# Performance work log

Hardware: AMD Instinct MI355X
Metric: run time of the kernel (lower is better)

The kernel has to match this reference:

```python
import jax, jax.numpy as jnp
import numpy as np

N_EXPERTS = 8
Z_DIM = 128
HID = 1024
OUT = 3072  # e.g. 3x32x32 flattened generator output
BATCH = 2048


def hash_vectors(z, n):
    """Deterministic per-sample hash -> expert index in [0, n).

    Proxy for the repo's hash_vectors (which hashes the latent vector):
    quantize |z|, sum over feature dim, mod n. Non-differentiable by design.
    """
    return jnp.mod(jnp.floor(jnp.abs(z) * 1000.0).sum(axis=1).astype(jnp.int32), n)


def setup_inputs() -> dict:
    key = jax.random.key(0)
    kz, k1, kb1, k2, kb2 = jax.random.split(key, 5)
    z = jax.random.normal(kz, (BATCH, Z_DIM), dtype=jnp.float32)
    s1 = 1.0 / np.sqrt(Z_DIM)
    s2 = 1.0 / np.sqrt(HID)
    # Stacked per-expert MLP params (each expert independently initialized,
    # mirroring reset_parameters on each deepcopy).
    W1 = jax.random.uniform(k1, (N_EXPERTS, Z_DIM, HID), jnp.float32, -s1, s1)
    b1 = jax.random.uniform(kb1, (N_EXPERTS, HID), jnp.float32, -s1, s1)
    W2 = jax.random.uniform(k2, (N_EXPERTS, HID, OUT), jnp.float32, -s2, s2)
    b2 = jax.random.uniform(kb2, (N_EXPERTS, OUT), jnp.float32, -s2, s2)
    return {"z": z, "W1": W1, "b1": b1, "W2": W2, "b2": b2}


def reference(z, W1, b1, W2, b2):
    # Hard routing: each sample i goes to expert idx[i].
    idx = hash_vectors(z, N_EXPERTS)  # [B]
    # Dense compute-all-experts then select (vectorized replacement for the
    # per-sample Python loop in the original forward).
    h = jax.nn.relu(jnp.einsum('bi,eih->beh', z, W1) + b1[None, :, :])  # [B,E,H]
    y = jnp.einsum('beh,eho->beo', h, W2) + b2[None, :, :]              # [B,E,O]
    out = jnp.take_along_axis(y, idx[:, None, None], axis=1)[:, 0, :]   # [B,O]
    return out
```

## Files before the change

kernel.cpp:

```cpp
#include <hip/hip_runtime.h>
#include <hip/hip_bf16.h>


#define BATCH 2048
#define ZD 128
#define HID 1024
#define OUTD 3072
#define NEXP 8

#define TMG 128
#define TNG 128
#define BKG 64
#define MAXTF 24

typedef short bf16x8 __attribute__((ext_vector_type(8)));
typedef float f32x4 __attribute__((ext_vector_type(4)));


__global__ __launch_bounds__(256) void route_kernel(const float* __restrict__ z,
                                                    __hip_bfloat16* __restrict__ zb,
                                                    int* counts, int* bucket) {
    __shared__ int lcnt[NEXP];
    __shared__ int gbase[NEXP];
    int t = threadIdx.x;
    if (t < NEXP) lcnt[t] = 0;
    __syncthreads();

    int s = blockIdx.x * 32 + (t >> 3);
    int li = t & 7;
    const float* zp = z + (size_t)s * ZD + li * 16;
    float sum = 0.f;
    union { bf16x8 v8; __hip_bfloat16 h[8]; } u0, u1;
#pragma unroll
    for (int i = 0; i < 4; i++) {
        float4 v = ((const float4*)zp)[i];
        sum += floorf(fabsf(v.x) * 1000.0f) + floorf(fabsf(v.y) * 1000.0f) +
               floorf(fabsf(v.z) * 1000.0f) + floorf(fabsf(v.w) * 1000.0f);
        __hip_bfloat16* dst = (i < 2) ? &u0.h[i * 4] : &u1.h[(i - 2) * 4];
        dst[0] = __float2bfloat16(v.x);
        dst[1] = __float2bfloat16(v.y);
        dst[2] = __float2bfloat16(v.z);
        dst[3] = __float2bfloat16(v.w);
    }
    bf16x8* zo = (bf16x8*)(zb + (size_t)s * ZD + li * 16);
    zo[0] = u0.v8;
    zo[1] = u1.v8;

    sum += __shfl_down(sum, 4);
    sum += __shfl_down(sum, 2);
    sum += __shfl_down(sum, 1);
    int e = 0, lpos = 0;
    if (li == 0) {
        e = ((int)sum) & 7;
        lpos = atomicAdd(&lcnt[e], 1);
    }
    __syncthreads();
    if (t < NEXP) gbase[t] = atomicAdd(&counts[t], lcnt[t]);
    __syncthreads();
    if (li == 0) bucket[e * BATCH + gbase[e] + lpos] = s;
}

__global__ void scan_kernel(const int* __restrict__ counts, int* ntl,
                            int* texp, int* perm, const int* __restrict__ bucket) {
    __shared__ int soff[NEXP + 1];
    __shared__ int scnt[NEXP];
    if (threadIdx.x == 0) {
        int o = 0;
        for (int e = 0; e < NEXP; e++) {
            scnt[e] = counts[e];
            soff[e] = o;
            o += (scnt[e] + TMG - 1) & ~(TMG - 1);
        }
        soff[NEXP] = o;
        *ntl = o / TMG;
    }
    __syncthreads();
    int total = soff[NEXP];
    for (int r = threadIdx.x; r < total; r += blockDim.x) {
        int e = 0;
        while (r >= soff[e + 1]) e++;
        int i = r - soff[e];
        perm[r] = (i < scnt[e]) ? bucket[e * BATCH + i] : -1;
        if ((r & (TMG - 1)) == 0) texp[r / TMG] = e;
    }
}

__global__ __launch_bounds__(256, 3) void gemm1_fast(
    const __hip_bfloat16* __restrict__ zb, const float* __restrict__ W1,
    const float* __restrict__ b1, const int* __restrict__ ntl,
    const int* __restrict__ texp, const int* __restrict__ perm,
    __hip_bfloat16* __restrict__ H) {
    int mt = blockIdx.y;
    if (mt >= *ntl) return;
    int e = texp[mt];
    int n0 = blockIdx.x * TNG;

    __shared__ __align__(16) __hip_bfloat16 As[TMG * BKG];
    __shared__ __align__(16) __hip_bfloat16 Bs[TNG * BKG];
    __shared__ int rows_s[TMG];

    int tid = threadIdx.x;
    if (tid < TMG) rows_s[tid] = perm[mt * TMG + tid];
    __syncthreads();

    int lane = tid & 63, wave = tid >> 6;
    int cc = lane & 15, q = lane >> 4;
    int mw = (wave >> 1) * 64, nw = (wave & 1) * 64;

    int sr = tid >> 3, sc = tid & 7;
    int awbase = sr * 64 + (sc ^ (sr & 7)) * 8;
    const __hip_bfloat16* Arp[4];
#pragma unroll
    for (int p = 0; p < 4; p++) {
        int r = rows_s[p * 32 + sr];
        if (r < 0) r = 0;
        Arp[p] = zb + (size_t)r * ZD + sc * 8;
    }
    int bkc = tid & 7, bn = (tid >> 3) * 4;
    const float* Bgf = W1 + (size_t)e * ZD * HID + (size_t)(bkc * 8) * HID + n0 + bn;
    int bwb[4];
#pragma unroll
    for (int j = 0; j < 4; j++)
        bwb[j] = (bn + j) * 64 + ((bkc ^ ((bn + j) & 7))) * 8;

    int A0 = (mw + cc) * 64, B0 = (nw + cc) * 64;
    int X0 = (q ^ (cc & 7)) * 8, X1 = ((4 + q) ^ (cc & 7)) * 8;

    float bias[4];
#pragma unroll
    for (int j = 0; j < 4; j++) bias[j] = b1[(size_t)e * HID + n0 + nw + j * 16 + cc];

    f32x4 zero4 = {0.f, 0.f, 0.f, 0.f};
    f32x4 acc[4][4];
#pragma unroll
    for (int i = 0; i < 4; i++)
#pragma unroll
        for (int j = 0; j < 4; j++) acc[i][j] = zero4;

    bf16x8 ga[4];
    union { bf16x8 v8; __hip_bfloat16 h[8]; } gb[4];
#pragma unroll
    for (int p = 0; p < 4; p++) ga[p] = *(const bf16x8*)(Arp[p]);
#pragma unroll
    for (int i = 0; i < 8; i++) {
        float4 v = *(const float4*)(Bgf + (size_t)i * HID);
        gb[0].h[i] = __float2bfloat16(v.x);
        gb[1].h[i] = __float2bfloat16(v.y);
        gb[2].h[i] = __float2bfloat16(v.z);
        gb[3].h[i] = __float2bfloat16(v.w);
    }
#pragma unroll
    for (int it = 0; it < ZD / BKG; ++it) {
        __syncthreads();
#pragma unroll
        for (int p = 0; p < 4; p++) *(bf16x8*)(As + awbase + p * 2048) = ga[p];
#pragma unroll
        for (int j = 0; j < 4; j++) *(bf16x8*)(Bs + bwb[j]) = gb[j].v8;
        __syncthreads();
        if (it + 1 < ZD / BKG) {
#pragma unroll
            for (int p = 0; p < 4; p++)
                ga[p] = *(const bf16x8*)(Arp[p] + (it + 1) * BKG);
#pragma unroll
            for (int i = 0; i < 8; i++) {
                float4 v = *(const float4*)(Bgf + (size_t)((it + 1) * BKG + i) * HID);
                gb[0].h[i] = __float2bfloat16(v.x);
                gb[1].h[i] = __float2bfloat16(v.y);
                gb[2].h[i] = __float2bfloat16(v.z);
                gb[3].h[i] = __float2bfloat16(v.w);
            }
        }
#pragma unroll
        for (int kh = 0; kh < 2; ++kh) {
            int X = kh ? X1 : X0;
            bf16x8 af[4], bfr[4];
#pragma unroll
            for (int i = 0; i < 4; i++) af[i] = *(const bf16x8*)(As + A0 + i * 1024 + X);
#pragma unroll
            for (int j = 0; j < 4; j++) bfr[j] = *(const bf16x8*)(Bs + B0 + j * 1024 + X);
#pragma unroll
            for (int i = 0; i < 4; i++)
#pragma unroll
                for (int j = 0; j < 4; j++)
                    acc[i][j] = __builtin_amdgcn_mfma_f32_16x16x32_bf16(af[i], bfr[j],
                                                                        acc[i][j], 0, 0, 0);
        }
    }
#pragma unroll
    for (int i = 0; i < 4; i++)
#pragma unroll
        for (int r = 0; r < 4; r++) {
            int m = mw + i * 16 + q * 4 + r;
            __hip_bfloat16* hp = H + (size_t)(mt * TMG + m) * HID + n0 + nw + cc;
#pragma unroll
            for (int j = 0; j < 4; j++)
                hp[j * 16] = __float2bfloat16(fmaxf(acc[i][j][r] + bias[j], 0.f));
        }
}

__global__ __launch_bounds__(256, 2) void gemm2_fast(
    const __hip_bfloat16* __restrict__ H, const float* __restrict__ W2,
    const float* __restrict__ b2, const int* __restrict__ ntl,
    const int* __restrict__ texp, const int* __restrict__ perm,
    float* __restrict__ out) {
    int mt = blockIdx.y;
    if (mt >= *ntl) return;
    int e = texp[mt];
    int n0 = blockIdx.x * TNG;

    __shared__ __align__(16) __hip_bfloat16 As[2][TMG * BKG];
    __shared__ __align__(16) __hip_bfloat16 Bs[2][TNG * BKG];
    __shared__ int rows_s[TMG];

    int tid = threadIdx.x;
    if (tid < TMG) rows_s[tid] = perm[mt * TMG + tid];

    int lane = tid & 63, wave = tid >> 6;
    int cc = lane & 15, q = lane >> 4;
    int mw = (wave >> 1) * 64, nw = (wave & 1) * 64;

    int sr = tid >> 3, sc = tid & 7;
    int awbase = sr * 64 + (sc ^ (sr & 7)) * 8;
    const __hip_bfloat16* Ag = H + ((size_t)mt * TMG + sr) * HID + sc * 8;
    int bkc = tid & 7, bn = (tid >> 3) * 4;
    const float* Bgf = W2 + (size_t)e * HID * OUTD + (size_t)(bkc * 8) * OUTD + n0 + bn;
    int bwb[4];
#pragma unroll
    for (int j = 0; j < 4; j++)
        bwb[j] = (bn + j) * 64 + ((bkc ^ ((bn + j) & 7))) * 8;

    int A0 = (mw + cc) * 64, B0 = (nw + cc) * 64;
    int X0 = (q ^ (cc & 7)) * 8, X1 = ((4 + q) ^ (cc & 7)) * 8;

    float bias[4];
#pragma unroll
    for (int j = 0; j < 4; j++) bias[j] = b2[(size_t)e * OUTD + n0 + nw + j * 16 + cc];

    f32x4 zero4 = {0.f, 0.f, 0.f, 0.f};
    f32x4 acc[4][4];
#pragma unroll
    for (int i = 0; i < 4; i++)
#pragma unroll
        for (int j = 0; j < 4; j++) acc[i][j] = zero4;

    bf16x8 ga[4];
    float4 braw[8];
#pragma unroll
    for (int p = 0; p < 4; p++) ga[p] = *(const bf16x8*)(Ag + (size_t)p * 32 * HID);
#pragma unroll
    for (int i = 0; i < 8; i++) braw[i] = *(const float4*)(Bgf + (size_t)i * OUTD);

    const int NIT = HID / BKG;
    for (int it = 0; it < NIT; ++it) {
        __hip_bfloat16* Ac = As[it & 1];
        __hip_bfloat16* Bc = Bs[it & 1];
        union { bf16x8 v8; __hip_bfloat16 h[8]; } gb[4];
#pragma unroll
        for (int i = 0; i < 8; i++) {
            gb[0].h[i] = __float2bfloat16(braw[i].x);
            gb[1].h[i] = __float2bfloat16(braw[i].y);
            gb[2].h[i] = __float2bfloat16(braw[i].z);
            gb[3].h[i] = __float2bfloat16(braw[i].w);
        }
#pragma unroll
        for (int p = 0; p < 4; p++) *(bf16x8*)(Ac + awbase + p * 2048) = ga[p];
#pragma unroll
        for (int j = 0; j < 4; j++) *(bf16x8*)(Bc + bwb[j]) = gb[j].v8;
        if (it + 1 < NIT) {
            int k1 = (it + 1) * BKG;
#pragma unroll
            for (int p = 0; p < 4; p++)
                ga[p] = *(const bf16x8*)(Ag + (size_t)p * 32 * HID + k1);
#pragma unroll
            for (int i = 0; i < 8; i++)
                braw[i] = *(const float4*)(Bgf + (size_t)(k1 + i) * OUTD);
        }
        __syncthreads();
#pragma unroll
        for (int kh = 0; kh < 2; ++kh) {
            int X = kh ? X1 : X0;
            bf16x8 af[4], bfr[4];
#pragma unroll
            for (int i = 0; i < 4; i++) af[i] = *(const bf16x8*)(Ac + A0 + i * 1024 + X);
#pragma unroll
            for (int j = 0; j < 4; j++) bfr[j] = *(const bf16x8*)(Bc + B0 + j * 1024 + X);
#pragma unroll
            for (int i = 0; i < 4; i++)
#pragma unroll
                for (int j = 0; j < 4; j++)
                    acc[i][j] = __builtin_amdgcn_mfma_f32_16x16x32_bf16(af[i], bfr[j],
                                                                        acc[i][j], 0, 0, 0);
        }
    }
#pragma unroll
    for (int i = 0; i < 4; i++)
#pragma unroll
        for (int r = 0; r < 4; r++) {
            int m = mw + i * 16 + q * 4 + r;
            int orow = rows_s[m];
            if (orow >= 0) {
                float* op = out + (size_t)orow * OUTD + n0 + nw + cc;
#pragma unroll
                for (int j = 0; j < 4; j++) op[j * 16] = acc[i][j][r] + bias[j];
            }
        }
}

extern "C" void kernel_launch(void* const* d_in, const int* in_sizes, int n_in,
                              void* d_out, int out_size, void* d_ws, size_t ws_size,
                              hipStream_t stream) {
    const float* z  = (const float*)d_in[0];
    const float* W1 = (const float*)d_in[1];
    const float* b1 = (const float*)d_in[2];
    const float* W2 = (const float*)d_in[3];
    const float* b2 = (const float*)d_in[4];
    float* out = (float*)d_out;

    char* ws = (char*)d_ws;
    int* counts = (int*)ws;
    int* ntl    = (int*)(ws + 64);
    int* texp   = (int*)(ws + 128);
    int* perm   = (int*)(ws + 256);
    int* bucket = (int*)(ws + 12544);
    __hip_bfloat16* zb  = (__hip_bfloat16*)(ws + 78080);
    __hip_bfloat16* Hb  = (__hip_bfloat16*)(ws + 602368);

    hipMemsetAsync(counts, 0, 64, stream);
    hipLaunchKernelGGL(route_kernel, dim3(BATCH / 32), dim3(256), 0, stream,
                       z, zb, counts, bucket);
    hipLaunchKernelGGL(scan_kernel, dim3(1), dim3(256), 0, stream,
                       counts, ntl, texp, perm, bucket);
    hipLaunchKernelGGL(gemm1_fast, dim3(HID / TNG, MAXTF), dim3(256), 0, stream,
                       zb, W1, b1, ntl, texp, perm, Hb);
    hipLaunchKernelGGL(gemm2_fast, dim3(OUTD / TNG, MAXTF), dim3(256), 0, stream,
                       Hb, W2, b2, ntl, texp, perm, out);
}
```

Before: 202.4 us.

## Deepen gemm2 global-load prefetch to two stages of register buffers

Restructures the gemm2 main loop to hold two sets of register prefetch buffers and issue global loads two K-iterations ahead, unrolling the loop by two via a macro. The aim is to hide more global memory latency behind MFMA work. It roughly doubles the registers used for prefetch (ga and braw), which under launch_bounds(256,2) may cause spills or lower occupancy.

```diff
diff --git a/kernel.cpp b/kernel.cpp
--- a/kernel.cpp
+++ b/kernel.cpp
@@ -198,6 +198,49 @@
         }
 }
 
+#define PIPE(S, IT)                                                            \
+    {                                                                          \
+        __hip_bfloat16* Ac = As[S];                                           \
+        __hip_bfloat16* Bc = Bs[S];                                           \
+        union { bf16x8 v8; __hip_bfloat16 h[8]; } gbv[4];                     \
+        _Pragma("unroll")                                                      \
+        for (int i = 0; i < 8; i++) {                                          \
+            gbv[0].h[i] = __float2bfloat16(braw[S][i].x);                      \
+            gbv[1].h[i] = __float2bfloat16(braw[S][i].y);                      \
+            gbv[2].h[i] = __float2bfloat16(braw[S][i].z);                      \
+            gbv[3].h[i] = __float2bfloat16(braw[S][i].w);                      \
+        }                                                                      \
+        _Pragma("unroll")                                                      \
+        for (int p = 0; p < 4; p++) *(bf16x8*)(Ac + awbase + p * 2048) = ga[S][p]; \
+        _Pragma("unroll")                                                      \
+        for (int j = 0; j < 4; j++) *(bf16x8*)(Bc + bwb[j]) = gbv[j].v8;       \
+        if ((IT) + 2 < NIT) {                                                  \
+            int k2 = ((IT) + 2) * BKG;                                         \
+            _Pragma("unroll")                                                  \
+            for (int p = 0; p < 4; p++)                                        \
+                ga[S][p] = *(const bf16x8*)(Ag + (size_t)p * 32 * HID + k2);   \
+            _Pragma("unroll")                                                  \
+            for (int i = 0; i < 8; i++)                                        \
+                braw[S][i] = *(const float4*)(Bgf + (size_t)(k2 + i) * OUTD);  \
+        }                                                                      \
+        __syncthreads();                                                       \
+        _Pragma("unroll")                                                      \
+        for (int kh = 0; kh < 2; ++kh) {                                       \
+            int X = kh ? X1 : X0;                                              \
+            bf16x8 af[4], bfr[4];                                              \
+            _Pragma("unroll")                                                  \
+            for (int i = 0; i < 4; i++) af[i] = *(const bf16x8*)(Ac + A0 + i * 1024 + X); \
+            _Pragma("unroll")                                                  \
+            for (int j = 0; j < 4; j++) bfr[j] = *(const bf16x8*)(Bc + B0 + j * 1024 + X); \
+            _Pragma("unroll")                                                  \
+            for (int i = 0; i < 4; i++)                                        \
+                _Pragma("unroll")                                              \
+                for (int j = 0; j < 4; j++)                                    \
+                    acc[i][j] = __builtin_amdgcn_mfma_f32_16x16x32_bf16(       \
+                        af[i], bfr[j], acc[i][j], 0, 0, 0);                    \
+        }                                                                      \
+    }
+
 __global__ __launch_bounds__(256, 2) void gemm2_fast(
     const __hip_bfloat16* __restrict__ H, const float* __restrict__ W2,
     const float* __restrict__ b2, const int* __restrict__ ntl,
@@ -243,55 +286,25 @@
 #pragma unroll
         for (int j = 0; j < 4; j++) acc[i][j] = zero4;
 
-    bf16x8 ga[4];
-    float4 braw[8];
-#pragma unroll
-    for (int p = 0; p < 4; p++) ga[p] = *(const bf16x8*)(Ag + (size_t)p * 32 * HID);
-#pragma unroll
-    for (int i = 0; i < 8; i++) braw[i] = *(const float4*)(Bgf + (size_t)i * OUTD);
-
     const int NIT = HID / BKG;
-    for (int it = 0; it < NIT; ++it) {
-        __hip_bfloat16* Ac = As[it & 1];
-        __hip_bfloat16* Bc = Bs[it & 1];
-        union { bf16x8 v8; __hip_bfloat16 h[8]; } gb[4];
-#pragma unroll
-        for (int i = 0; i < 8; i++) {
-            gb[0].h[i] = __float2bfloat16(braw[i].x);
-            gb[1].h[i] = __float2bfloat16(braw[i].y);
-            gb[2].h[i] = __float2bfloat16(braw[i].z);
-            gb[3].h[i] = __float2bfloat16(braw[i].w);
-        }
-#pragma unroll
-        for (int p = 0; p < 4; p++) *(bf16x8*)(Ac + awbase + p * 2048) = ga[p];
-#pragma unroll
-        for (int j = 0; j < 4; j++) *(bf16x8*)(Bc + bwb[j]) = gb[j].v8;
-        if (it + 1 < NIT) {
-            int k1 = (it + 1) * BKG;
-#pragma unroll
-            for (int p = 0; p < 4; p++)
-                ga[p] = *(const bf16x8*)(Ag + (size_t)p * 32 * HID + k1);
-#pragma unroll
-            for (int i = 0; i < 8; i++)
-                braw[i] = *(const float4*)(Bgf + (size_t)(k1 + i) * OUTD);
-        }
-        __syncthreads();
-#pragma unroll
-        for (int kh = 0; kh < 2; ++kh) {
-            int X = kh ? X1 : X0;
-            bf16x8 af[4], bfr[4];
-#pragma unroll
-            for (int i = 0; i < 4; i++) af[i] = *(const bf16x8*)(Ac + A0 + i * 1024 + X);
-#pragma unroll
-            for (int j = 0; j < 4; j++) bfr[j] = *(const bf16x8*)(Bc + B0 + j * 1024 + X);
-#pragma unroll
-            for (int i = 0; i < 4; i++)
-#pragma unroll
-                for (int j = 0; j < 4; j++)
-                    acc[i][j] = __builtin_amdgcn_mfma_f32_16x16x32_bf16(af[i], bfr[j],
-                                                                        acc[i][j], 0, 0, 0);
-        }
-    }
+
+    bf16x8 ga[2][4];
+    float4 braw[2][8];
+#pragma unroll
+    for (int s = 0; s < 2; s++) {
+#pragma unroll
+        for (int p = 0; p < 4; p++)
+            ga[s][p] = *(const bf16x8*)(Ag + (size_t)p * 32 * HID + s * BKG);
+#pragma unroll
+        for (int i = 0; i < 8; i++)
+            braw[s][i] = *(const float4*)(Bgf + (size_t)(s * BKG + i) * OUTD);
+    }
+
+    for (int it = 0; it < NIT; it += 2) {
+        PIPE(0, it);
+        PIPE(1, it + 1);
+    }
+
 #pragma unroll
     for (int i = 0; i < 4; i++)
 #pragma unroll
```

New measurement: 203.9 us. About the same (+0.7%).

## Shrink GEMM N tiles, warp-specialize loaders, double-buffer gemm1 shared memory

Applied to the files above, without the earlier changes.

Both grouped GEMMs use narrower N tiles: 32 columns for gemm1 and 64 for gemm2. This launches more blocks so more of the GPU is busy given the small routed M. Loading is split by wave: some waves fetch and convert W to bf16 while others fetch the gathered activations. gemm1 also gets double-buffered shared memory, and the occupancy hints are raised. The cost is more redundant A reloads, since each A tile is now fetched by more blocks, plus lower MFMA reuse per block and idle waves during loads.

```diff
diff --git a/kernel.cpp b/kernel.cpp
--- a/kernel.cpp
+++ b/kernel.cpp
@@ -7,10 +7,6 @@
 #define HID 1024
 #define OUTD 3072
 #define NEXP 8
-
-#define TMG 128
-#define TNG 128
-#define BKG 64
 #define MAXTF 24
 
 typedef short bf16x8 __attribute__((ext_vector_type(8)));
@@ -69,10 +65,10 @@
         for (int e = 0; e < NEXP; e++) {
             scnt[e] = counts[e];
             soff[e] = o;
-            o += (scnt[e] + TMG - 1) & ~(TMG - 1);
+            o += (scnt[e] + 127) & ~127;
         }
         soff[NEXP] = o;
-        *ntl = o / TMG;
+        *ntl = o / 128;
     }
     __syncthreads();
     int total = soff[NEXP];
@@ -81,11 +77,11 @@
         while (r >= soff[e + 1]) e++;
         int i = r - soff[e];
         perm[r] = (i < scnt[e]) ? bucket[e * BATCH + i] : -1;
-        if ((r & (TMG - 1)) == 0) texp[r / TMG] = e;
-    }
-}
-
-__global__ __launch_bounds__(256, 3) void gemm1_fast(
+        if ((r & 127) == 0) texp[r / 128] = e;
+    }
+}
+
+__global__ __launch_bounds__(256, 4) void gemm1_fast(
     const __hip_bfloat16* __restrict__ zb, const float* __restrict__ W1,
     const float* __restrict__ b1, const int* __restrict__ ntl,
     const int* __restrict__ texp, const int* __restrict__ perm,
@@ -93,97 +89,102 @@
     int mt = blockIdx.y;
     if (mt >= *ntl) return;
     int e = texp[mt];
-    int n0 = blockIdx.x * TNG;
-
-    __shared__ __align__(16) __hip_bfloat16 As[TMG * BKG];
-    __shared__ __align__(16) __hip_bfloat16 Bs[TNG * BKG];
-    __shared__ int rows_s[TMG];
+    int n0 = blockIdx.x * 32;
+
+    __shared__ __align__(16) __hip_bfloat16 As[2][128 * 64];
+    __shared__ __align__(16) __hip_bfloat16 Bs[2][32 * 64];
+    __shared__ int rows_s[128];
 
     int tid = threadIdx.x;
-    if (tid < TMG) rows_s[tid] = perm[mt * TMG + tid];
+    if (tid < 128) rows_s[tid] = perm[mt * 128 + tid];
     __syncthreads();
 
     int lane = tid & 63, wave = tid >> 6;
     int cc = lane & 15, q = lane >> 4;
-    int mw = (wave >> 1) * 64, nw = (wave & 1) * 64;
-
-    int sr = tid >> 3, sc = tid & 7;
-    int awbase = sr * 64 + (sc ^ (sr & 7)) * 8;
-    const __hip_bfloat16* Arp[4];
-#pragma unroll
-    for (int p = 0; p < 4; p++) {
-        int r = rows_s[p * 32 + sr];
+    int mw = (wave >> 1) * 64, nw = (wave & 1) * 16;
+
+    bool isB = (wave == 0);
+    bool isA = (wave >= 2);
+    int bkc = tid & 7, bn = ((tid >> 3) & 7) * 4;
+    const float* Bgf = W1 + (size_t)e * ZD * HID + (size_t)(bkc * 8) * HID + n0 + bn;
+    int bwb[4];
+#pragma unroll
+    for (int j = 0; j < 4; j++)
+        bwb[j] = ((bn + j) * 8 + (bkc ^ ((bn + j) & 7))) * 8;
+    int t2 = tid & 127;
+    int sc = t2 & 7, rg = t2 >> 3;
+    const __hip_bfloat16* Arp[8];
+#pragma unroll
+    for (int p = 0; p < 8; p++) {
+        int r = rows_s[rg + 16 * p];
         if (r < 0) r = 0;
         Arp[p] = zb + (size_t)r * ZD + sc * 8;
     }
-    int bkc = tid & 7, bn = (tid >> 3) * 4;
-    const float* Bgf = W1 + (size_t)e * ZD * HID + (size_t)(bkc * 8) * HID + n0 + bn;
-    int bwb[4];
-#pragma unroll
-    for (int j = 0; j < 4; j++)
-        bwb[j] = (bn + j) * 64 + ((bkc ^ ((bn + j) & 7))) * 8;
+    int awb = rg * 64 + (sc ^ (rg & 7)) * 8;
 
     int A0 = (mw + cc) * 64, B0 = (nw + cc) * 64;
     int X0 = (q ^ (cc & 7)) * 8, X1 = ((4 + q) ^ (cc & 7)) * 8;
 
-    float bias[4];
-#pragma unroll
-    for (int j = 0; j < 4; j++) bias[j] = b1[(size_t)e * HID + n0 + nw + j * 16 + cc];
+    float bias = b1[(size_t)e * HID + n0 + nw + cc];
 
     f32x4 zero4 = {0.f, 0.f, 0.f, 0.f};
-    f32x4 acc[4][4];
-#pragma unroll
-    for (int i = 0; i < 4; i++)
-#pragma unroll
-        for (int j = 0; j < 4; j++) acc[i][j] = zero4;
-
-    bf16x8 ga[4];
-    union { bf16x8 v8; __hip_bfloat16 h[8]; } gb[4];
-#pragma unroll
-    for (int p = 0; p < 4; p++) ga[p] = *(const bf16x8*)(Arp[p]);
-#pragma unroll
-    for (int i = 0; i < 8; i++) {
-        float4 v = *(const float4*)(Bgf + (size_t)i * HID);
-        gb[0].h[i] = __float2bfloat16(v.x);
-        gb[1].h[i] = __float2bfloat16(v.y);
-        gb[2].h[i] = __float2bfloat16(v.z);
-        gb[3].h[i] = __float2bfloat16(v.w);
-    }
-#pragma unroll
-    for (int it = 0; it < ZD / BKG; ++it) {
+    f32x4 acc[4];
+#pragma unroll
+    for (int i = 0; i < 4; i++) acc[i] = zero4;
+
+    float4 braw[8];
+    bf16x8 ga[8];
+    if (isB) {
+#pragma unroll
+        for (int i = 0; i < 8; i++) braw[i] = *(const float4*)(Bgf + (size_t)i * HID);
+    } else if (isA) {
+#pragma unroll
+        for (int p = 0; p < 8; p++) ga[p] = *(const bf16x8*)(Arp[p]);
+    }
+
+    const int NIT = ZD / 64;
+#pragma unroll
+    for (int it = 0; it < NIT; ++it) {
+        __hip_bfloat16* Ac = As[it & 1];
+        __hip_bfloat16* Bc = Bs[it & 1];
+        if (isB) {
+            union { bf16x8 v8; __hip_bfloat16 h[8]; } gbv[4];
+#pragma unroll
+            for (int i = 0; i < 8; i++) {
+                gbv[0].h[i] = __float2bfloat16(braw[i].x);
+                gbv[1].h[i] = __float2bfloat16(braw[i].y);
+                gbv[2].h[i] = __float2bfloat16(braw[i].z);
+                gbv[3].h[i] = __float2bfloat16(braw[i].w);
+            }
+#pragma unroll
+            for (int j = 0; j < 4; j++) *(bf16x8*)(Bc + bwb[j]) = gbv[j].v8;
+        } else if (isA) {
+#pragma unroll
+            for (int p = 0; p < 8; p++) *(bf16x8*)(Ac + awb + p * 1024) = ga[p];
+        }
+        if (it + 1 < NIT) {
+            int k1 = (it + 1) * 64;
+            if (isB) {
+#pragma unroll
+                for (int i = 0; i < 8; i++)
+                    braw[i] = *(const float4*)(Bgf + (size_t)(k1 + i) * HID);
+            } else if (isA) {
+#pragma unroll
+                for (int p = 0; p < 8; p++) ga[p] = *(const bf16x8*)(Arp[p] + k1);
+            }
+        }
         __syncthreads();
-#pragma unroll
-        for (int p = 0; p < 4; p++) *(bf16x8*)(As + awbase + p * 2048) = ga[p];
-#pragma unroll
-        for (int j = 0; j < 4; j++) *(bf16x8*)(Bs + bwb[j]) = gb[j].v8;
-        __syncthreads();
-        if (it + 1 < ZD / BKG) {
-#pragma unroll
-            for (int p = 0; p < 4; p++)
-                ga[p] = *(const bf16x8*)(Arp[p] + (it + 1) * BKG);
-#pragma unroll
-            for (int i = 0; i < 8; i++) {
-                float4 v = *(const float4*)(Bgf + (size_t)((it + 1) * BKG + i) * HID);
-                gb[0].h[i] = __float2bfloat16(v.x);
-                gb[1].h[i] = __float2bfloat16(v.y);
-                gb[2].h[i] = __float2bfloat16(v.z);
-                gb[3].h[i] = __float2bfloat16(v.w);
-            }
-        }
 #pragma unroll
         for (int kh = 0; kh < 2; ++kh) {
             int X = kh ? X1 : X0;
-            bf16x8 af[4], bfr[4];
-#pragma unroll
-            for (int i = 0; i < 4; i++) af[i] = *(const bf16x8*)(As + A0 + i * 1024 + X);
-#pragma unroll
-            for (int j = 0; j < 4; j++) bfr[j] = *(const bf16x8*)(Bs + B0 + j * 1024 + X);
+            bf16x8 af[4], bfr;
+#pragma unroll
+            for (int i = 0; i < 4; i++) af[i] = *(const bf16x8*)(Ac + A0 + i * 1024 + X);
+            bfr = *(const bf16x8*)(Bc + B0 + X);
 #pragma unroll
             for (int i = 0; i < 4; i++)
-#pragma unroll
-                for (int j = 0; j < 4; j++)
-                    acc[i][j] = __builtin_amdgcn_mfma_f32_16x16x32_bf16(af[i], bfr[j],
-                                                                        acc[i][j], 0, 0, 0);
+                acc[i] = __builtin_amdgcn_mfma_f32_16x16x32_bf16(af[i], bfr,
+                                                                 acc[i], 0, 0, 0);
         }
     }
 #pragma unroll
@@ -191,14 +192,12 @@
 #pragma unroll
         for (int r = 0; r < 4; r++) {
             int m = mw + i * 16 + q * 4 + r;
-            __hip_bfloat16* hp = H + (size_t)(mt * TMG + m) * HID + n0 + nw + cc;
-#pragma unroll
-            for (int j = 0; j < 4; j++)
-                hp[j * 16] = __float2bfloat16(fmaxf(acc[i][j][r] + bias[j], 0.f));
-        }
-}
-
-__global__ __launch_bounds__(256, 2) void gemm2_fast(
+            H[(size_t)(mt * 128 + m) * HID + n0 + nw + cc] =
+                __float2bfloat16(fmaxf(acc[i][r] + bias, 0.f));
+        }
+}
+
+__global__ __launch_bounds__(256, 3) void gemm2_fast(
     const __hip_bfloat16* __restrict__ H, const float* __restrict__ W2,
     const float* __restrict__ b2, const int* __restrict__ ntl,
     const int* __restrict__ texp, const int* __restrict__ perm,
@@ -206,88 +205,98 @@
     int mt = blockIdx.y;
     if (mt >= *ntl) return;
     int e = texp[mt];
-    int n0 = blockIdx.x * TNG;
-
-    __shared__ __align__(16) __hip_bfloat16 As[2][TMG * BKG];
-    __shared__ __align__(16) __hip_bfloat16 Bs[2][TNG * BKG];
-    __shared__ int rows_s[TMG];
+    int n0 = blockIdx.x * 64;
+
+    __shared__ __align__(16) __hip_bfloat16 As[2][128 * 64];
+    __shared__ __align__(16) __hip_bfloat16 Bs[2][64 * 64];
+    __shared__ int rows_s[128];
 
     int tid = threadIdx.x;
-    if (tid < TMG) rows_s[tid] = perm[mt * TMG + tid];
-
+    if (tid < 128) rows_s[tid] = perm[mt * 128 + tid];
     int lane = tid & 63, wave = tid >> 6;
     int cc = lane & 15, q = lane >> 4;
-    int mw = (wave >> 1) * 64, nw = (wave & 1) * 64;
-
-    int sr = tid >> 3, sc = tid & 7;
-    int awbase = sr * 64 + (sc ^ (sr & 7)) * 8;
-    const __hip_bfloat16* Ag = H + ((size_t)mt * TMG + sr) * HID + sc * 8;
-    int bkc = tid & 7, bn = (tid >> 3) * 4;
+    int mw = (wave >> 1) * 64, nw = (wave & 1) * 32;
+
+    bool isB = (wave < 2);
+    int bkc = tid & 7, bn = ((tid >> 3) & 15) * 4;
     const float* Bgf = W2 + (size_t)e * HID * OUTD + (size_t)(bkc * 8) * OUTD + n0 + bn;
     int bwb[4];
 #pragma unroll
     for (int j = 0; j < 4; j++)
-        bwb[j] = (bn + j) * 64 + ((bkc ^ ((bn + j) & 7))) * 8;
+        bwb[j] = ((bn + j) * 8 + (bkc ^ ((bn + j) & 7))) * 8;
+    int t2 = tid & 127;
+    int sc = t2 & 7, rg = t2 >> 3;
+    const __hip_bfloat16* Ag = H + ((size_t)mt * 128 + rg) * HID + sc * 8;
+    int awb = rg * 64 + (sc ^ (rg & 7)) * 8;
 
     int A0 = (mw + cc) * 64, B0 = (nw + cc) * 64;
     int X0 = (q ^ (cc & 7)) * 8, X1 = ((4 + q) ^ (cc & 7)) * 8;
 
-    float bias[4];
-#pragma unroll
-    for (int j = 0; j < 4; j++) bias[j] = b2[(size_t)e * OUTD + n0 + nw + j * 16 + cc];
+    float bias[2];
+#pragma unroll
+    for (int j = 0; j < 2; j++) bias[j] = b2[(size_t)e * OUTD + n0 + nw + j * 16 + cc];
 
     f32x4 zero4 = {0.f, 0.f, 0.f, 0.f};
-    f32x4 acc[4][4];
+    f32x4 acc[4][2];
 #pragma unroll
     for (int i = 0; i < 4; i++)
 #pragma unroll
-        for (int j = 0; j < 4; j++) acc[i][j] = zero4;
-
-    bf16x8 ga[4];
+        for (int j = 0; j < 2; j++) acc[i][j] = zero4;
+
     float4 braw[8];
-#pragma unroll
-    for (int p = 0; p < 4; p++) ga[p] = *(const bf16x8*)(Ag + (size_t)p * 32 * HID);
-#pragma unroll
-    for (int i = 0; i < 8; i++) braw[i] = *(const float4*)(Bgf + (size_t)i * OUTD);
-
-    const int NIT = HID / BKG;
+    bf16x8 ga[8];
+    if (isB) {
+#pragma unroll
+        for (int i = 0; i < 8; i++) braw[i] = *(const float4*)(Bgf + (size_t)i * OUTD);
+    } else {
+#pragma unroll
+        for (int p = 0; p < 8; p++) ga[p] = *(const bf16x8*)(Ag + (size_t)p * 16 * HID);
+    }
+
+    const int NIT = HID / 64;
     for (int it = 0; it < NIT; ++it) {
         __hip_bfloat16* Ac = As[it & 1];
         __hip_bfloat16* Bc = Bs[it & 1];
-        union { bf16x8 v8; __hip_bfloat16 h[8]; } gb[4];
-#pragma unroll
-        for (int i = 0; i < 8; i++) {
-            gb[0].h[i] = __float2bfloat16(braw[i].x);
-            gb[1].h[i] = __float2bfloat16(braw[i].y);
-            gb[2].h[i] = __float2bfloat16(braw[i].z);
-            gb[3].h[i] = __float2bfloat16(braw[i].w);
-        }
-#pragma unroll
-        for (int p = 0; p < 4; p++) *(bf16x8*)(Ac + awbase + p * 2048) = ga[p];
-#pragma unroll
-        for (int j = 0; j < 4; j++) *(bf16x8*)(Bc + bwb[j]) = gb[j].v8;
+        if (isB) {
+            union { bf16x8 v8; __hip_bfloat16 h[8]; } gbv[4];
+#pragma unroll
+            for (int i = 0; i < 8; i++) {
+                gbv[0].h[i] = __float2bfloat16(braw[i].x);
+                gbv[1].h[i] = __float2bfloat16(braw[i].y);
+                gbv[2].h[i] = __float2bfloat16(braw[i].z);
+                gbv[3].h[i] = __float2bfloat16(braw[i].w);
+            }
+#pragma unroll
+            for (int j = 0; j < 4; j++) *(bf16x8*)(Bc + bwb[j]) = gbv[j].v8;
+        } else {
+#pragma unroll
+            for (int p = 0; p < 8; p++) *(bf16x8*)(Ac + awb + p * 1024) = ga[p];
+        }
         if (it + 1 < NIT) {
-            int k1 = (it + 1) * BKG;
-#pragma unroll
-            for (int p = 0; p < 4; p++)
-                ga[p] = *(const bf16x8*)(Ag + (size_t)p * 32 * HID + k1);
-#pragma unroll
-            for (int i = 0; i < 8; i++)
-                braw[i] = *(const float4*)(Bgf + (size_t)(k1 + i) * OUTD);
+            int k1 = (it + 1) * 64;
+            if (isB) {
+#pragma unroll
+                for (int i = 0; i < 8; i++)
+                    braw[i] = *(const float4*)(Bgf + (size_t)(k1 + i) * OUTD);
+            } else {
+#pragma unroll
+                for (int p = 0; p < 8; p++)
+                    ga[p] = *(const bf16x8*)(Ag + (size_t)p * 16 * HID + k1);
+            }
         }
         __syncthreads();
 #pragma unroll
         for (int kh = 0; kh < 2; ++kh) {
             int X = kh ? X1 : X0;
-            bf16x8 af[4], bfr[4];
+            bf16x8 af[4], bfr[2];
 #pragma unroll
             for (int i = 0; i < 4; i++) af[i] = *(const bf16x8*)(Ac + A0 + i * 1024 + X);
 #pragma unroll
-            for (int j = 0; j < 4; j++) bfr[j] = *(const bf16x8*)(Bc + B0 + j * 1024 + X);
+            for (int j = 0; j < 2; j++) bfr[j] = *(const bf16x8*)(Bc + B0 + j * 1024 + X);
 #pragma unroll
             for (int i = 0; i < 4; i++)
 #pragma unroll
-                for (int j = 0; j < 4; j++)
+                for (int j = 0; j < 2; j++)
                     acc[i][j] = __builtin_amdgcn_mfma_f32_16x16x32_bf16(af[i], bfr[j],
                                                                         acc[i][j], 0, 0, 0);
         }
@@ -301,7 +310,7 @@
             if (orow >= 0) {
                 float* op = out + (size_t)orow * OUTD + n0 + nw + cc;
 #pragma unroll
-                for (int j = 0; j < 4; j++) op[j * 16] = acc[i][j][r] + bias[j];
+                for (int j = 0; j < 2; j++) op[j * 16] = acc[i][j][r] + bias[j];
             }
         }
 }
@@ -330,8 +339,8 @@
                        z, zb, counts, bucket);
     hipLaunchKernelGGL(scan_kernel, dim3(1), dim3(256), 0, stream,
                        counts, ntl, texp, perm, bucket);
-    hipLaunchKernelGGL(gemm1_fast, dim3(HID / TNG, MAXTF), dim3(256), 0, stream,
+    hipLaunchKernelGGL(gemm1_fast, dim3(HID / 32, MAXTF), dim3(256), 0, stream,
                        zb, W1, b1, ntl, texp, perm, Hb);
-    hipLaunchKernelGGL(gemm2_fast, dim3(OUTD / TNG, MAXTF), dim3(256), 0, stream,
+    hipLaunchKernelGGL(gemm2_fast, dim3(OUTD / 64, MAXTF), dim3(256), 0, stream,
                        Hb, W2, b2, ntl, texp, perm, out);
 }
```

Result: slower. 210.9 us (+4.2%).
